# Optimization experiments

Measured on AMD Instinct MI355X. Metric: run time of the kernel, lower is better.

Reference implementation:

```python
import jax, jax.numpy as jnp
import numpy as np

B, D_INNER, D_STATE, D_ATTN = 1024, 4096, 16, 16
SCALE = D_ATTN ** (-0.5)


def setup_inputs() -> dict:
    key = jax.random.key(0)
    k1, k2, k3, k4 = jax.random.split(key, 4)
    h = jax.random.normal(k1, (B, D_INNER, D_STATE), dtype=jnp.float32)
    W_q = jax.random.normal(k2, (D_ATTN, D_INNER), dtype=jnp.float32) * (D_INNER ** -0.5)
    W_k = jax.random.normal(k3, (D_ATTN, D_INNER), dtype=jnp.float32) * (D_INNER ** -0.5)
    # gate is zero-initialized in the module; use a small random scalar so the
    # attention branch is exercised in correctness testing.
    gate = jax.random.normal(k4, (1,), dtype=jnp.float32) * 0.1
    return {"h": h, "W_q": W_q, "W_k": W_k, "gate": gate}


def reference(h, W_q, W_k, gate):
    # h: (B, d_inner, d_state) -> slots: (B, d_state, d_inner)
    slots = jnp.swapaxes(h, 1, 2)
    q = jnp.einsum("bsd,ad->bsa", slots, W_q)  # (B, d_state, d_attn)
    k = jnp.einsum("bsd,ad->bsa", slots, W_k)  # (B, d_state, d_attn)
    attn = jax.nn.softmax(jnp.einsum("bsa,bta->bst", q, k) * SCALE, axis=-1)
    out = jnp.einsum("bst,btd->bsd", attn, slots)  # (B, d_state, d_inner)
    out = jnp.swapaxes(out, 1, 2)  # back to (B, d_inner, d_state)
    return h + gate[0] * out
```

## Files before the change

kernel.cpp:

```cpp
#include <hip/hip_runtime.h>
#include <hip/hip_bf16.h>


constexpr int DI = 4096;
constexpr int DS = 16;
constexpr int NW = 8;

typedef __attribute__((ext_vector_type(8))) short bf16x8;
typedef __attribute__((ext_vector_type(4))) float f32x4;

static __device__ __forceinline__ short f2bf(float x) {
    union { __hip_bfloat16 h; short s; } u;
    u.h = __float2bfloat16(x);
    return u.s;
}

__global__ __launch_bounds__(512, 4) void ica_fused(
    const float* __restrict__ h,
    const float* __restrict__ Wq,
    const float* __restrict__ Wk,
    const float* __restrict__ gate,
    float* __restrict__ out)
{
    const int b    = blockIdx.x;
    const int tid  = threadIdx.x;
    const int lane = tid & 63;
    const int wv   = tid >> 6;

    const float* __restrict__ hbase = h   + (size_t)b * (DI * DS);
    float*       __restrict__ obase = out + (size_t)b * (DI * DS);

    __shared__ float qp[NW][16][20];
    __shared__ float kp[NW][16][20];
    __shared__ float Qs[16][20];
    __shared__ float Ks[16][20];
    __shared__ float Ms[16][20];

    const int sa = lane & 15;
    const int kb = lane >> 4;

    {
        constexpr int ROWS = DI / NW;
        constexpr int NIT  = ROWS / 32;
        const int d0w = wv * ROWS;
        const float* __restrict__ wqb = Wq + (size_t)sa * DI;
        const float* __restrict__ wkb = Wk + (size_t)sa * DI;

        f32x4 accQ = {0.f, 0.f, 0.f, 0.f};
        f32x4 accK = {0.f, 0.f, 0.f, 0.f};

        float  F[8];
        float4 FQ0, FQ1, FK0, FK1;
        bf16x8 afr, bqr, bkr;

#define P1_LDF(IT) do {                                                     \
        const int db_ = d0w + (IT) * 32 + kb * 8;                           \
        const float* __restrict__ hp_ = hbase + (size_t)db_ * DS + sa;      \
        F[0] = hp_[0 * DS]; F[1] = hp_[1 * DS];                             \
        F[2] = hp_[2 * DS]; F[3] = hp_[3 * DS];                             \
        F[4] = hp_[4 * DS]; F[5] = hp_[5 * DS];                             \
        F[6] = hp_[6 * DS]; F[7] = hp_[7 * DS];                             \
        FQ0 = *(const float4*)(wqb + db_); FQ1 = *(const float4*)(wqb + db_ + 4); \
        FK0 = *(const float4*)(wkb + db_); FK1 = *(const float4*)(wkb + db_ + 4); \
    } while (0)

#define P1_CVT() do {                                                       \
        afr[0] = f2bf(F[0]); afr[1] = f2bf(F[1]);                           \
        afr[2] = f2bf(F[2]); afr[3] = f2bf(F[3]);                           \
        afr[4] = f2bf(F[4]); afr[5] = f2bf(F[5]);                           \
        afr[6] = f2bf(F[6]); afr[7] = f2bf(F[7]);                           \
        bqr[0] = f2bf(FQ0.x); bqr[1] = f2bf(FQ0.y);                         \
        bqr[2] = f2bf(FQ0.z); bqr[3] = f2bf(FQ0.w);                         \
        bqr[4] = f2bf(FQ1.x); bqr[5] = f2bf(FQ1.y);                         \
        bqr[6] = f2bf(FQ1.z); bqr[7] = f2bf(FQ1.w);                         \
        bkr[0] = f2bf(FK0.x); bkr[1] = f2bf(FK0.y);                         \
        bkr[2] = f2bf(FK0.z); bkr[3] = f2bf(FK0.w);                         \
        bkr[4] = f2bf(FK1.x); bkr[5] = f2bf(FK1.y);                         \
        bkr[6] = f2bf(FK1.z); bkr[7] = f2bf(FK1.w);                         \
    } while (0)

        P1_LDF(0);
        for (int it = 0; it < NIT - 1; ++it) {
            P1_CVT();
            P1_LDF(it + 1);
            accQ = __builtin_amdgcn_mfma_f32_16x16x32_bf16(afr, bqr, accQ, 0, 0, 0);
            accK = __builtin_amdgcn_mfma_f32_16x16x32_bf16(afr, bkr, accK, 0, 0, 0);
        }
        P1_CVT();
        accQ = __builtin_amdgcn_mfma_f32_16x16x32_bf16(afr, bqr, accQ, 0, 0, 0);
        accK = __builtin_amdgcn_mfma_f32_16x16x32_bf16(afr, bkr, accK, 0, 0, 0);
#undef P1_LDF
#undef P1_CVT

        #pragma unroll
        for (int r = 0; r < 4; ++r) {
            qp[wv][kb * 4 + r][sa] = accQ[r];
            kp[wv][kb * 4 + r][sa] = accK[r];
        }
    }
    __syncthreads();

    {
        const int idx = tid & 255;
        const int s2 = idx >> 4, a2 = idx & 15;
        if (tid < 256) {
            float q = 0.f;
            #pragma unroll
            for (int w = 0; w < NW; ++w) q += qp[w][s2][a2];
            Qs[s2][a2] = q;
        } else {
            float k = 0.f;
            #pragma unroll
            for (int w = 0; w < NW; ++w) k += kp[w][s2][a2];
            Ks[s2][a2] = k;
        }
    }
    __syncthreads();

    const float g = gate[0];
    if (tid < 256) {
        const int ss = tid >> 4;
        const int tt = tid & 15;
        float sc = 0.f;
        #pragma unroll
        for (int a4 = 0; a4 < 16; a4 += 4) {
            float4 qv = *(const float4*)&Qs[ss][a4];
            float4 kv = *(const float4*)&Ks[tt][a4];
            sc = fmaf(qv.x, kv.x, sc);
            sc = fmaf(qv.y, kv.y, sc);
            sc = fmaf(qv.z, kv.z, sc);
            sc = fmaf(qv.w, kv.w, sc);
        }
        sc *= 0.25f;

        float m = sc;
        #pragma unroll
        for (int o = 8; o > 0; o >>= 1) m = fmaxf(m, __shfl_xor(m, o, 16));
        float e = __expf(sc - m);
        float sm = e;
        #pragma unroll
        for (int o = 8; o > 0; o >>= 1) sm += __shfl_xor(sm, o, 16);
        Ms[ss][tt] = g * (e / sm);
    }
    __syncthreads();

    {
        constexpr int ROWS = DI / NW;
        constexpr int NT3  = ROWS / 16;
        const int rbase = wv * ROWS;
        const int row  = lane >> 2;
        const int quad = lane & 3;

        float (* __restrict__ st)[20] = qp[wv];

        bf16x8 bfrag = {0, 0, 0, 0, 0, 0, 0, 0};
        if (kb < 2) {
            const float* mp = &Ms[sa][kb * 8];
            float4 m0 = *(const float4*)mp;
            float4 m1 = *(const float4*)(mp + 4);
            bfrag[0] = f2bf(m0.x); bfrag[1] = f2bf(m0.y);
            bfrag[2] = f2bf(m0.z); bfrag[3] = f2bf(m0.w);
            bfrag[4] = f2bf(m1.x); bfrag[5] = f2bf(m1.y);
            bfrag[6] = f2bf(m1.z); bfrag[7] = f2bf(m1.w);
        }

        float4 hn = *(const float4*)(hbase + (size_t)(rbase + row) * DS + quad * 4);

        for (int it = 0; it < NT3; ++it) {
            const float4 hres = hn;
            *(float4*)&st[row][quad * 4] = hres;
            if (it + 1 < NT3)
                hn = *(const float4*)(hbase + (size_t)(rbase + (it + 1) * 16 + row) * DS + quad * 4);
            __builtin_amdgcn_wave_barrier();

            const float* ap = &st[sa][(kb & 1) * 8];
            float4 aa0 = *(const float4*)ap;
            float4 aa1 = *(const float4*)(ap + 4);
            if (kb >= 2) {
                aa0 = make_float4(0.f, 0.f, 0.f, 0.f);
                aa1 = make_float4(0.f, 0.f, 0.f, 0.f);
            }
            bf16x8 af;
            af[0] = f2bf(aa0.x); af[1] = f2bf(aa0.y);
            af[2] = f2bf(aa0.z); af[3] = f2bf(aa0.w);
            af[4] = f2bf(aa1.x); af[5] = f2bf(aa1.y);
            af[6] = f2bf(aa1.z); af[7] = f2bf(aa1.w);

            f32x4 acc = {0.f, 0.f, 0.f, 0.f};
            acc = __builtin_amdgcn_mfma_f32_16x16x32_bf16(af, bfrag, acc, 0, 0, 0);
            __builtin_amdgcn_wave_barrier();

            #pragma unroll
            for (int r = 0; r < 4; ++r)
                st[kb * 4 + r][sa] = acc[r];
            __builtin_amdgcn_wave_barrier();

            float4 pv = *(const float4*)&st[row][quad * 4];
            f32x4 o;
            o[0] = hres.x + pv.x;
            o[1] = hres.y + pv.y;
            o[2] = hres.z + pv.z;
            o[3] = hres.w + pv.w;
            const size_t orow = (size_t)(rbase + it * 16 + row) * DS + quad * 4;
            __builtin_nontemporal_store(o, (f32x4*)(obase + orow));
            __builtin_amdgcn_wave_barrier();
        }
    }
}

extern "C" void kernel_launch(void* const* d_in, const int* in_sizes, int n_in,
                              void* d_out, int out_size, void* d_ws, size_t ws_size,
                              hipStream_t stream) {
    const float* h    = (const float*)d_in[0];
    const float* Wq   = (const float*)d_in[1];
    const float* Wk   = (const float*)d_in[2];
    const float* gate = (const float*)d_in[3];
    float* out = (float*)d_out;
    (void)in_sizes; (void)n_in; (void)out_size; (void)d_ws; (void)ws_size;

    ica_fused<<<1024, 512, 0, stream>>>(h, Wq, Wk, gate, out);
}
```

Measured before the change: 144.9 us.

## Keep h tile in registers across both passes to avoid re-reading global memory

Each wave now loads its 512x16 slice of h once, with coalesced float4 loads, into 32 float4 registers. That slice feeds both the Q/K projection (transposed through LDS for the MFMA A operand) and the residual/output pass, so the second global read of h and the strided scalar loads of the first pass are removed. Launch bounds drop to one block per CU-slot hint to allow the large register footprint, which can lower occupancy and latency hiding. A triple-buffered W prefetch is kept.

```diff
diff --git a/kernel.cpp b/kernel.cpp
--- a/kernel.cpp
+++ b/kernel.cpp
@@ -15,7 +15,7 @@
     return u.s;
 }
 
-__global__ __launch_bounds__(512, 4) void ica_fused(
+__global__ __launch_bounds__(512, 1) void ica_fused(
     const float* __restrict__ h,
     const float* __restrict__ Wq,
     const float* __restrict__ Wk,
@@ -30,67 +30,76 @@
     const float* __restrict__ hbase = h   + (size_t)b * (DI * DS);
     float*       __restrict__ obase = out + (size_t)b * (DI * DS);
 
+    __shared__ float st[NW][32][20];
     __shared__ float qp[NW][16][20];
     __shared__ float kp[NW][16][20];
     __shared__ float Qs[16][20];
     __shared__ float Ks[16][20];
     __shared__ float Ms[16][20];
 
-    const int sa = lane & 15;
-    const int kb = lane >> 4;
+    const int sa   = lane & 15;
+    const int kb   = lane >> 4;
+    const int row  = lane >> 2;
+    const int quad = lane & 3;
+
+    const float4* __restrict__ h4 = (const float4*)hbase + (size_t)wv * 2048;
+    const int d0w = wv * 512;
+
+    float4 H[32];
 
     {
-        constexpr int ROWS = DI / NW;
-        constexpr int NIT  = ROWS / 32;
-        const int d0w = wv * ROWS;
         const float* __restrict__ wqb = Wq + (size_t)sa * DI;
         const float* __restrict__ wkb = Wk + (size_t)sa * DI;
 
         f32x4 accQ = {0.f, 0.f, 0.f, 0.f};
         f32x4 accK = {0.f, 0.f, 0.f, 0.f};
 
-        float  F[8];
-        float4 FQ0, FQ1, FK0, FK1;
-        bf16x8 afr, bqr, bkr;
-
-#define P1_LDF(IT) do {                                                     \
-        const int db_ = d0w + (IT) * 32 + kb * 8;                           \
-        const float* __restrict__ hp_ = hbase + (size_t)db_ * DS + sa;      \
-        F[0] = hp_[0 * DS]; F[1] = hp_[1 * DS];                             \
-        F[2] = hp_[2 * DS]; F[3] = hp_[3 * DS];                             \
-        F[4] = hp_[4 * DS]; F[5] = hp_[5 * DS];                             \
-        F[6] = hp_[6 * DS]; F[7] = hp_[7 * DS];                             \
-        FQ0 = *(const float4*)(wqb + db_); FQ1 = *(const float4*)(wqb + db_ + 4); \
-        FK0 = *(const float4*)(wkb + db_); FK1 = *(const float4*)(wkb + db_ + 4); \
+        float4 WQ0[3], WQ1[3], WK0[3], WK1[3];
+
+#define LD_CHUNK(C, SL) do {                                                \
+        H[2*(C)]   = h4[(2*(C)) * 64 + lane];                               \
+        H[2*(C)+1] = h4[(2*(C)+1) * 64 + lane];                             \
+        const int db_ = d0w + (C) * 32 + kb * 8;                            \
+        WQ0[SL] = *(const float4*)(wqb + db_);                              \
+        WQ1[SL] = *(const float4*)(wqb + db_ + 4);                          \
+        WK0[SL] = *(const float4*)(wkb + db_);                              \
+        WK1[SL] = *(const float4*)(wkb + db_ + 4);                          \
     } while (0)
 
-#define P1_CVT() do {                                                       \
-        afr[0] = f2bf(F[0]); afr[1] = f2bf(F[1]);                           \
-        afr[2] = f2bf(F[2]); afr[3] = f2bf(F[3]);                           \
-        afr[4] = f2bf(F[4]); afr[5] = f2bf(F[5]);                           \
-        afr[6] = f2bf(F[6]); afr[7] = f2bf(F[7]);                           \
-        bqr[0] = f2bf(FQ0.x); bqr[1] = f2bf(FQ0.y);                         \
-        bqr[2] = f2bf(FQ0.z); bqr[3] = f2bf(FQ0.w);                         \
-        bqr[4] = f2bf(FQ1.x); bqr[5] = f2bf(FQ1.y);                         \
-        bqr[6] = f2bf(FQ1.z); bqr[7] = f2bf(FQ1.w);                         \
-        bkr[0] = f2bf(FK0.x); bkr[1] = f2bf(FK0.y);                         \
-        bkr[2] = f2bf(FK0.z); bkr[3] = f2bf(FK0.w);                         \
-        bkr[4] = f2bf(FK1.x); bkr[5] = f2bf(FK1.y);                         \
-        bkr[6] = f2bf(FK1.z); bkr[7] = f2bf(FK1.w);                         \
-    } while (0)
-
-        P1_LDF(0);
-        for (int it = 0; it < NIT - 1; ++it) {
-            P1_CVT();
-            P1_LDF(it + 1);
-            accQ = __builtin_amdgcn_mfma_f32_16x16x32_bf16(afr, bqr, accQ, 0, 0, 0);
-            accK = __builtin_amdgcn_mfma_f32_16x16x32_bf16(afr, bkr, accK, 0, 0, 0);
-        }
-        P1_CVT();
-        accQ = __builtin_amdgcn_mfma_f32_16x16x32_bf16(afr, bqr, accQ, 0, 0, 0);
-        accK = __builtin_amdgcn_mfma_f32_16x16x32_bf16(afr, bkr, accK, 0, 0, 0);
-#undef P1_LDF
-#undef P1_CVT
+        LD_CHUNK(0, 0);
+        LD_CHUNK(1, 1);
+        LD_CHUNK(2, 2);
+
+        #pragma unroll
+        for (int c = 0; c < 16; ++c) {
+            const int sl = c % 3;
+            *(float4*)&st[wv][row][quad * 4]      = H[2*c];
+            *(float4*)&st[wv][row + 16][quad * 4] = H[2*c + 1];
+
+            bf16x8 bq, bk;
+            bq[0] = f2bf(WQ0[sl].x); bq[1] = f2bf(WQ0[sl].y);
+            bq[2] = f2bf(WQ0[sl].z); bq[3] = f2bf(WQ0[sl].w);
+            bq[4] = f2bf(WQ1[sl].x); bq[5] = f2bf(WQ1[sl].y);
+            bq[6] = f2bf(WQ1[sl].z); bq[7] = f2bf(WQ1[sl].w);
+            bk[0] = f2bf(WK0[sl].x); bk[1] = f2bf(WK0[sl].y);
+            bk[2] = f2bf(WK0[sl].z); bk[3] = f2bf(WK0[sl].w);
+            bk[4] = f2bf(WK1[sl].x); bk[5] = f2bf(WK1[sl].y);
+            bk[6] = f2bf(WK1[sl].z); bk[7] = f2bf(WK1[sl].w);
+
+            __builtin_amdgcn_wave_barrier();
+
+            if (c + 3 < 16) LD_CHUNK(c + 3, sl);
+
+            bf16x8 af;
+            #pragma unroll
+            for (int i = 0; i < 8; ++i)
+                af[i] = f2bf(st[wv][kb * 8 + i][sa]);
+
+            accQ = __builtin_amdgcn_mfma_f32_16x16x32_bf16(af, bq, accQ, 0, 0, 0);
+            accK = __builtin_amdgcn_mfma_f32_16x16x32_bf16(af, bk, accK, 0, 0, 0);
+            __builtin_amdgcn_wave_barrier();
+        }
+#undef LD_CHUNK
 
         #pragma unroll
         for (int r = 0; r < 4; ++r) {
@@ -145,13 +154,7 @@
     __syncthreads();
 
     {
-        constexpr int ROWS = DI / NW;
-        constexpr int NT3  = ROWS / 16;
-        const int rbase = wv * ROWS;
-        const int row  = lane >> 2;
-        const int quad = lane & 3;
-
-        float (* __restrict__ st)[20] = qp[wv];
+        float (* __restrict__ stw)[20] = st[wv];
 
         bf16x8 bfrag = {0, 0, 0, 0, 0, 0, 0, 0};
         if (kb < 2) {
@@ -164,16 +167,12 @@
             bfrag[6] = f2bf(m1.z); bfrag[7] = f2bf(m1.w);
         }
 
-        float4 hn = *(const float4*)(hbase + (size_t)(rbase + row) * DS + quad * 4);
-
-        for (int it = 0; it < NT3; ++it) {
-            const float4 hres = hn;
-            *(float4*)&st[row][quad * 4] = hres;
-            if (it + 1 < NT3)
-                hn = *(const float4*)(hbase + (size_t)(rbase + (it + 1) * 16 + row) * DS + quad * 4);
-            __builtin_amdgcn_wave_barrier();
-
-            const float* ap = &st[sa][(kb & 1) * 8];
+        #pragma unroll
+        for (int it = 0; it < 32; ++it) {
+            *(float4*)&stw[row][quad * 4] = H[it];
+            __builtin_amdgcn_wave_barrier();
+
+            const float* ap = &stw[sa][(kb & 1) * 8];
             float4 aa0 = *(const float4*)ap;
             float4 aa1 = *(const float4*)(ap + 4);
             if (kb >= 2) {
@@ -192,16 +191,16 @@
 
             #pragma unroll
             for (int r = 0; r < 4; ++r)
-                st[kb * 4 + r][sa] = acc[r];
-            __builtin_amdgcn_wave_barrier();
-
-            float4 pv = *(const float4*)&st[row][quad * 4];
+                stw[kb * 4 + r][sa] = acc[r];
+            __builtin_amdgcn_wave_barrier();
+
+            float4 pv = *(const float4*)&stw[row][quad * 4];
             f32x4 o;
-            o[0] = hres.x + pv.x;
-            o[1] = hres.y + pv.y;
-            o[2] = hres.z + pv.z;
-            o[3] = hres.w + pv.w;
-            const size_t orow = (size_t)(rbase + it * 16 + row) * DS + quad * 4;
+            o[0] = H[it].x + pv.x;
+            o[1] = H[it].y + pv.y;
+            o[2] = H[it].z + pv.z;
+            o[3] = H[it].w + pv.w;
+            const size_t orow = (size_t)(d0w + it * 16 + row) * DS + quad * 4;
             __builtin_nontemporal_store(o, (f32x4*)(obase + orow));
             __builtin_amdgcn_wave_barrier();
         }
```

New measurement: 117.1 us (median of 2 runs). -19.2%, faster.
